# Kernel optimization log

Measured on AMD Instinct MI355X. Metric: run time of the kernel, lower is better.

The kernel has to match this reference:

```python
import jax, jax.numpy as jnp
import numpy as np

B, S, H, NH = 2, 2048, 1024, 16
DK = H // NH

def setup_inputs() -> dict:
    key = jax.random.key(0)
    ks = jax.random.split(key, 12)
    scale = 0.02
    return {
        "Q": jax.random.normal(ks[0], (B, S, H), jnp.float32),
        "K": jax.random.normal(ks[1], (B, S, H), jnp.float32),
        "V": jax.random.normal(ks[2], (B, S, H), jnp.float32),
        "attn_mask": jax.random.randint(ks[3], (B, S, S), 0, 2).astype(bool),
        "Wq": jax.random.normal(ks[4], (H, H), jnp.float32) * scale,
        "bq": jnp.zeros((H,), jnp.float32),
        "Wk": jax.random.normal(ks[5], (H, H), jnp.float32) * scale,
        "bk": jnp.zeros((H,), jnp.float32),
        "Wv": jax.random.normal(ks[6], (H, H), jnp.float32) * scale,
        "bv": jnp.zeros((H,), jnp.float32),
        "Wo": jax.random.normal(ks[7], (H, H), jnp.float32) * scale,
        "bo": jnp.zeros((H,), jnp.float32),
    }

def reference(Q, K, V, attn_mask, Wq, bq, Wk, bk, Wv, bv, Wo, bo):
    b = Q.shape[0]
    # linear projections (torch nn.Linear: x @ W.T + b), split heads -> [b, nh, s, dk]
    def proj(x, W, bias):
        return (x @ W.T + bias).reshape(b, -1, NH, DK).transpose(0, 2, 1, 3)
    q = proj(Q, Wq, bq)
    k = proj(K, Wk, bk)
    v = proj(V, Wv, bv)
    scores = jnp.einsum("bhqd,bhkd->bhqk", q, k) / jnp.sqrt(jnp.float32(DK))
    scores = jnp.where(attn_mask[:, None, :, :], jnp.float32(-1e9), scores)
    attn = jax.nn.softmax(scores, axis=-1)  # dropout prob = 0.0 (identity)
    ctx = jnp.einsum("bhqk,bhkd->bhqd", attn, v)
    ctx = ctx.transpose(0, 2, 1, 3).reshape(b, -1, NH * DK)
    return ctx @ Wo.T + bo
```

## Files before the change

kernel.cpp:

```cpp
#include <hip/hip_runtime.h>
#include <hip/hip_bf16.h>

typedef short s16x8 __attribute__((ext_vector_type(8)));
typedef float f32x4 __attribute__((ext_vector_type(4)));
typedef unsigned short u16;
typedef unsigned int u32;
typedef unsigned long long u64;

#define DEVI __device__ __forceinline__

#if __has_builtin(__builtin_amdgcn_exp2f)
#define EXP2F(x) __builtin_amdgcn_exp2f(x)
#else
#define EXP2F(x) exp2f(x)
#endif

#define QSCALE 0.1803368801111204f

DEVI float bf2f(u16 u){ union { u32 i; float f; } v; v.i = ((u32)u) << 16; return v.f; }
DEVI u16 f2bf(float f){ union { float f; u32 i; } v; v.f = f; u32 u = v.i;
                        return (u16)((u + 0x7fffu + ((u >> 16) & 1u)) >> 16); }

DEVI u32 pkbf2(float a, float b){
  union { __hip_bfloat162 h; u32 u; } v;
  v.h = __float22bfloat162_rn(make_float2(a, b));
  return v.u;
}
DEVI u64 pk4(float a, float b, float c, float d){
  return (u64)pkbf2(a, b) | ((u64)pkbf2(c, d) << 32);
}

DEVI f32x4 mfma_bf16(s16x8 a, s16x8 b, f32x4 c){
  return __builtin_amdgcn_mfma_f32_16x16x32_bf16(a, b, c, 0, 0, 0);
}

#define GLDS(gp, lp) __builtin_amdgcn_global_load_lds( \
    (const __attribute__((address_space(1))) void*)(gp), \
    (__attribute__((address_space(3))) void*)(lp), 16, 0, 0)

DEVI float4 cvt8f32(const float* p){
  float4 x = *(const float4*)p;
  float4 y = *(const float4*)(p + 4);
  union { u32 t[4]; float4 f4; } u;
  u.t[0] = pkbf2(x.x, x.y); u.t[1] = pkbf2(x.z, x.w);
  u.t[2] = pkbf2(y.x, y.y); u.t[3] = pkbf2(y.z, y.w);
  return u.f4;
}

DEVI bool detect_f32(const u16* probe){
  __shared__ int dsum[4];
  const int tid = threadIdx.x;
  int bad = 0;
#pragma unroll
  for (int i = 0; i < 16; ++i){
    u16 u = probe[tid * 16 + i];
    int e = (u >> 7) & 0xFF;
    bad += (e != 0 && (e < 100 || e > 150)) ? 1 : 0;
  }
#pragma unroll
  for (int o = 1; o < 64; o <<= 1) bad += __shfl_xor(bad, o);
  if ((tid & 63) == 0) dsum[tid >> 6] = bad;
  __syncthreads();
  bool r = (dsum[0] + dsum[1] + dsum[2] + dsum[3]) > 64;
  __syncthreads();
  return r;
}

struct PrepArgs { const void* src[7]; void* dst[7]; u32 coff[8]; };

__global__ __launch_bounds__(256) void prep_mask(PrepArgs a, const u16* probe,
                                                 const int* __restrict__ mask,
                                                 u64* __restrict__ bits,
                                                 int do_mask, int do_conv){
  if (blockIdx.x < 1024){
    if (!do_mask) return;
    const int lane = threadIdx.x & 63, wid = threadIdx.x >> 6;
    const int row = blockIdx.x * 4 + wid;
    const int* mrow = mask + (size_t)row * 2048;
    for (int c = 0; c < 32; ++c){
      int v = mrow[c * 64 + lane];
      u64 w = __ballot(v == 0);
      if (lane == 0) bits[(size_t)row * 32 + c] = w;
    }
  } else {
    if (!do_conv) return;
    const bool f32 = detect_f32(probe);
    if (!f32) return;
    const u32 total = a.coff[7];
    for (u32 c = (blockIdx.x - 1024) * 256 + threadIdx.x; c < total; c += 2048 * 256){
      int s = 0;
#pragma unroll
      for (int i = 1; i < 7; ++i) s += (c >= a.coff[i]) ? 1 : 0;
      u32 lc = c - a.coff[s];
      ((float4*)a.dst[s])[lc] = cvt8f32((const float*)a.src[s] + (size_t)lc * 8);
    }
  }
}

struct ProjP {
  const void* X[3];   const u16* Xc[3];
  const void* W[3];   const u16* Wc[3];
  const void* bias[3];
  u16* out[3];
  const u16* probe;
  int conv_ok;
};

__global__ __launch_bounds__(256) void proj_gemm(ProjP p){
  __shared__ u16 As[128 * 64];
  __shared__ u16 Bs[128 * 64];
  const int z = blockIdx.z;
  const bool in32 = detect_f32(p.probe);
  const bool f32st = in32 && !p.conv_ok;
  const u16* Ab = (in32 && p.conv_ok) ? p.Xc[z] : (const u16*)p.X[z];
  const u16* Wb = (in32 && p.conv_ok) ? p.Wc[z] : (const u16*)p.W[z];
  const float* Af = (const float*)p.X[z];
  const float* Wf = (const float*)p.W[z];
  const int tid = threadIdx.x;
  const int lane = tid & 63, wid = tid >> 6;
  const int quad = lane >> 4, l15 = lane & 15;
  const int m0 = blockIdx.y * 128, n0 = blockIdx.x * 128;
  const int wm = (wid >> 1) * 64, wn = (wid & 1) * 64;
  const int K = 1024;

  f32x4 acc[4][4];
  const f32x4 z4 = {0.f, 0.f, 0.f, 0.f};
  for (int i = 0; i < 4; ++i) for (int j = 0; j < 4; ++j) acc[i][j] = z4;

  for (int ko = 0; ko < 16; ++ko){
    const int kk = ko * 64;
    if (f32st){
#pragma unroll
      for (int i = 0; i < 4; ++i){
        int g = tid * 4 + i;
        int row = g >> 3, c = g & 7;
        *(float4*)(As + row * 64 + ((c ^ (row & 7)) * 8)) =
            cvt8f32(Af + (size_t)(m0 + row) * K + kk + c * 8);
        *(float4*)(Bs + row * 64 + ((c ^ (row & 7)) * 8)) =
            cvt8f32(Wf + (size_t)(n0 + row) * K + kk + c * 8);
      }
    } else {
#pragma unroll
      for (int i = 0; i < 4; ++i){
        int ci = (wid * 4 + i) * 64 + lane;
        int row = ci >> 3, gcc = (ci & 7) ^ (row & 7);
        GLDS(Ab + (size_t)(m0 + row) * K + kk + gcc * 8, As + (size_t)(wid * 4 + i) * 512);
        GLDS(Wb + (size_t)(n0 + row) * K + kk + gcc * 8, Bs + (size_t)(wid * 4 + i) * 512);
      }
    }
    __syncthreads();
#pragma unroll
    for (int ks = 0; ks < 2; ++ks){
      s16x8 af[4], bfr[4];
#pragma unroll
      for (int mt = 0; mt < 4; ++mt){
        int row = wm + mt * 16 + l15;
        af[mt] = *(const s16x8*)(As + row * 64 + (((ks * 4 + quad) ^ (row & 7)) * 8));
      }
#pragma unroll
      for (int nt = 0; nt < 4; ++nt){
        int row = wn + nt * 16 + l15;
        bfr[nt] = *(const s16x8*)(Bs + row * 64 + (((ks * 4 + quad) ^ (row & 7)) * 8));
      }
#pragma unroll
      for (int mt = 0; mt < 4; ++mt)
#pragma unroll
        for (int nt = 0; nt < 4; ++nt)
          acc[mt][nt] = mfma_bf16(af[mt], bfr[nt], acc[mt][nt]);
    }
    __syncthreads();
  }

  u16* outp = p.out[z];
#pragma unroll
  for (int nt = 0; nt < 4; ++nt){
    int col = n0 + wn + nt * 16 + l15;
    float bv = in32 ? ((const float*)p.bias[z])[col] : bf2f(((const u16*)p.bias[z])[col]);
#pragma unroll
    for (int mt = 0; mt < 4; ++mt){
      if (z == 2){
        int srow = m0 + wm + mt * 16 + quad * 4;
        int b = srow >> 11, s = srow & 2047, hh = col >> 6, d = col & 63;
        size_t idx = (((size_t)(b * 16 + hh)) * 64 + d) * 2048 + s;
        *(u64*)(outp + idx) = pk4(acc[mt][nt][0] + bv, acc[mt][nt][1] + bv,
                                  acc[mt][nt][2] + bv, acc[mt][nt][3] + bv);
      } else {
#pragma unroll
        for (int r = 0; r < 4; ++r){
          int row = m0 + wm + mt * 16 + quad * 4 + r;
          float v = acc[mt][nt][r] + bv;
          if (z == 0) v *= QSCALE;
          int b = row >> 11, s = row & 2047, hh = col >> 6, d = col & 63;
          outp[(((size_t)(b * 16 + hh)) * 2048 + s) * 64 + d] = f2bf(v);
        }
      }
    }
  }
}

__global__ __launch_bounds__(256) void gemm_out(const u16* __restrict__ A,
                                                const void* __restrict__ Wv,
                                                const u16* __restrict__ Wbf,
                                                const void* __restrict__ biasv,
                                                void* __restrict__ outv,
                                                const u16* __restrict__ probe,
                                                int conv_ok){
  __shared__ u16 As[64 * 64];
  __shared__ u16 Bs[64 * 64];
  const bool in32 = detect_f32(probe);
  const bool f32st = in32 && !conv_ok;
  const u16* Wb = (in32 && conv_ok) ? Wbf : (const u16*)Wv;
  const float* Wf = (const float*)Wv;
  const int tid = threadIdx.x;
  const int lane = tid & 63, wid = tid >> 6;
  const int quad = lane >> 4, l15 = lane & 15;
  const int m0 = blockIdx.y * 64, n0 = blockIdx.x * 64;
  const int wm = (wid >> 1) * 32, wn = (wid & 1) * 32;
  const int K = 1024;

  f32x4 acc[2][2];
  const f32x4 z4 = {0.f, 0.f, 0.f, 0.f};
  for (int i = 0; i < 2; ++i) for (int j = 0; j < 2; ++j) acc[i][j] = z4;

  for (int ko = 0; ko < 16; ++ko){
    const int kk = ko * 64;
#pragma unroll
    for (int i = 0; i < 2; ++i){
      int ci = (wid * 2 + i) * 64 + lane;
      int row = ci >> 3, gcc = (ci & 7) ^ (row & 7);
      GLDS(A + (size_t)(m0 + row) * K + kk + gcc * 8, As + (size_t)(wid * 2 + i) * 512);
    }
    if (f32st){
#pragma unroll
      for (int i = 0; i < 2; ++i){
        int g = tid * 2 + i;
        int row = g >> 3, c = g & 7;
        *(float4*)(Bs + row * 64 + ((c ^ (row & 7)) * 8)) =
            cvt8f32(Wf + (size_t)(n0 + row) * K + kk + c * 8);
      }
    } else {
#pragma unroll
      for (int i = 0; i < 2; ++i){
        int ci = (wid * 2 + i) * 64 + lane;
        int row = ci >> 3, gcc = (ci & 7) ^ (row & 7);
        GLDS(Wb + (size_t)(n0 + row) * K + kk + gcc * 8, Bs + (size_t)(wid * 2 + i) * 512);
      }
    }
    __syncthreads();
#pragma unroll
    for (int ks = 0; ks < 2; ++ks){
      s16x8 af[2], bfr[2];
#pragma unroll
      for (int mt = 0; mt < 2; ++mt){
        int row = wm + mt * 16 + l15;
        af[mt] = *(const s16x8*)(As + row * 64 + (((ks * 4 + quad) ^ (row & 7)) * 8));
      }
#pragma unroll
      for (int nt = 0; nt < 2; ++nt){
        int row = wn + nt * 16 + l15;
        bfr[nt] = *(const s16x8*)(Bs + row * 64 + (((ks * 4 + quad) ^ (row & 7)) * 8));
      }
#pragma unroll
      for (int mt = 0; mt < 2; ++mt)
#pragma unroll
        for (int nt = 0; nt < 2; ++nt)
          acc[mt][nt] = mfma_bf16(af[mt], bfr[nt], acc[mt][nt]);
    }
    __syncthreads();
  }

#pragma unroll
  for (int nt = 0; nt < 2; ++nt){
    int col = n0 + wn + nt * 16 + l15;
    float bv = in32 ? ((const float*)biasv)[col] : bf2f(((const u16*)biasv)[col]);
#pragma unroll
    for (int mt = 0; mt < 2; ++mt)
#pragma unroll
      for (int r = 0; r < 4; ++r){
        int row = m0 + wm + mt * 16 + quad * 4 + r;
        float v = acc[mt][nt][r] + bv;
        size_t idx = (size_t)row * 1024 + col;
        if (in32) ((float*)outv)[idx] = v;
        else      ((u16*)outv)[idx]   = f2bf(v);
      }
  }
}

__global__ __launch_bounds__(256) void attn2(const u16* __restrict__ qws,
                                             const u16* __restrict__ kws,
                                             const u16* __restrict__ vtws,
                                             const u64* __restrict__ mbits,
                                             const int* __restrict__ rawmask,
                                             int use_raw,
                                             u16* __restrict__ ctxws){
  __shared__ u16 Ks[2][64 * 64];
  __shared__ u16 Vt[2][64 * 64];
  __shared__ u16 Ps[4][16 * 64];
  const int tid = threadIdx.x;
  const int lane = tid & 63, wid = tid >> 6;
  const int quad = lane >> 4, l15 = lane & 15;
  const int h = blockIdx.x, qt = blockIdx.y, b = blockIdx.z;
  const int q0 = qt * 64;
  const size_t bh = (size_t)(b * 16 + h) * (2048 * 64);
  const int qrow = q0 + wid * 16 + l15;

  s16x8 qf[2];
#pragma unroll
  for (int ks = 0; ks < 2; ++ks)
    qf[ks] = *(const s16x8*)(qws + bh + (size_t)qrow * 64 + ks * 32 + quad * 8);

  const f32x4 z4 = {0.f, 0.f, 0.f, 0.f};
  f32x4 ctx[4];
  for (int dt = 0; dt < 4; ++dt) ctx[dt] = z4;
  float lr = 0.f;

  u16* pp = &Ps[wid][0];
  u32 pw[4];
#pragma unroll
  for (int ntk = 0; ntk < 4; ++ntk)
    pw[ntk] = l15 * 64 + (((u32)(ntk * 2 + (quad >> 1)) ^ (u32)(l15 & 7)) * 8) + (quad & 1) * 4;

  const u64* mrow = mbits + ((size_t)(b * 2048 + qrow)) * 32;

  const int sci = wid * 2;
  int srow0, sgc0, srow1, sgc1;
  {
    int ci0 = sci * 64 + lane;
    srow0 = ci0 >> 3; sgc0 = (ci0 & 7) ^ (srow0 & 7);
    int ci1 = (sci + 1) * 64 + lane;
    srow1 = ci1 >> 3; sgc1 = (ci1 & 7) ^ (srow1 & 7);
  }

  {
    const int k0 = 0;
    GLDS(kws + bh + (size_t)(k0 + srow0) * 64 + sgc0 * 8, &Ks[0][0] + (size_t)sci * 512);
    GLDS(vtws + bh + (size_t)srow0 * 2048 + k0 + sgc0 * 8, &Vt[0][0] + (size_t)sci * 512);
    GLDS(kws + bh + (size_t)(k0 + srow1) * 64 + sgc1 * 8, &Ks[0][0] + (size_t)(sci + 1) * 512);
    GLDS(vtws + bh + (size_t)srow1 * 2048 + k0 + sgc1 * 8, &Vt[0][0] + (size_t)(sci + 1) * 512);
  }

  for (int kt = 0; kt < 32; ++kt){
    const int cur = kt & 1;
    const u16* kb = &Ks[cur][0];
    const u16* vb = &Vt[cur][0];
    __syncthreads();

    u64 mw = 0;
    if (!use_raw) mw = mrow[kt];

    if (kt < 31){
      const int k0n = (kt + 1) * 64;
      u16* kd = &Ks[cur ^ 1][0];
      u16* vd = &Vt[cur ^ 1][0];
      GLDS(kws + bh + (size_t)(k0n + srow0) * 64 + sgc0 * 8, kd + (size_t)sci * 512);
      GLDS(vtws + bh + (size_t)srow0 * 2048 + k0n + sgc0 * 8, vd + (size_t)sci * 512);
      GLDS(kws + bh + (size_t)(k0n + srow1) * 64 + sgc1 * 8, kd + (size_t)(sci + 1) * 512);
      GLDS(vtws + bh + (size_t)srow1 * 2048 + k0n + sgc1 * 8, vd + (size_t)(sci + 1) * 512);
    }

    const int k0 = kt * 64;

    f32x4 s[4];
    for (int ntk = 0; ntk < 4; ++ntk) s[ntk] = z4;
#pragma unroll
    for (int ks = 0; ks < 2; ++ks)
#pragma unroll
      for (int ntk = 0; ntk < 4; ++ntk){
        int row = ntk * 16 + l15;
        s16x8 kf = *(const s16x8*)(kb + row * 64 + (((ks * 4 + quad) ^ (row & 7)) * 8));
        s[ntk] = mfma_bf16(kf, qf[ks], s[ntk]);
      }

    float ls = 0.f;
    if (!use_raw){
      u64 w = mw >> (quad * 4);
      u32 wlo = (u32)w, whi = (u32)(w >> 32);
#pragma unroll
      for (int ntk = 0; ntk < 4; ++ntk){
        u32 half = (ntk < 2) ? wlo : whi;
#pragma unroll
        for (int r = 0; r < 4; ++r){
          u32 keep = half & (1u << ((ntk & 1) * 16 + r));
          float sv = keep ? s[ntk][r] : -1.0e9f;
          float pv = EXP2F(sv);
          s[ntk][r] = pv;
          ls += pv;
        }
      }
    } else {
#pragma unroll
      for (int ntk = 0; ntk < 4; ++ntk)
#pragma unroll
        for (int r = 0; r < 4; ++r){
          int key = k0 + ntk * 16 + quad * 4 + r;
          int mv = rawmask[((size_t)(b * 2048 + qrow)) * 2048 + key];
          float pv = EXP2F(mv ? -1.0e9f : s[ntk][r]);
          s[ntk][r] = pv;
          ls += pv;
        }
    }
    lr += ls;

#pragma unroll
    for (int ntk = 0; ntk < 4; ++ntk){
      uint2 t;
      t.x = pkbf2(s[ntk][0], s[ntk][1]);
      t.y = pkbf2(s[ntk][2], s[ntk][3]);
      *(uint2*)(pp + pw[ntk]) = t;
    }
    s16x8 pf[2];
#pragma unroll
    for (int ks = 0; ks < 2; ++ks)
      pf[ks] = *(const s16x8*)(pp + l15 * 64 + (((ks * 4 + quad) ^ (l15 & 7)) * 8));

#pragma unroll
    for (int ks = 0; ks < 2; ++ks)
#pragma unroll
      for (int dt = 0; dt < 4; ++dt){
        int row = dt * 16 + l15;
        s16x8 vf = *(const s16x8*)(vb + row * 64 + (((ks * 4 + quad) ^ (row & 7)) * 8));
        ctx[dt] = mfma_bf16(vf, pf[ks], ctx[dt]);
      }
  }

  lr += __shfl_xor(lr, 16);
  lr += __shfl_xor(lr, 32);
  float inv = 1.0f / fmaxf(lr, 1e-30f);

#pragma unroll
  for (int dt = 0; dt < 4; ++dt){
    int d0 = dt * 16 + quad * 4;
    u64 w = pk4(ctx[dt][0] * inv, ctx[dt][1] * inv, ctx[dt][2] * inv, ctx[dt][3] * inv);
    *(u64*)(ctxws + ((size_t)(b * 2048 + qrow)) * 1024 + h * 64 + d0) = w;
  }
}

extern "C" void kernel_launch(void* const* d_in, const int* in_sizes, int n_in,
                              void* d_out, int out_size, void* d_ws, size_t ws_size,
                              hipStream_t stream){
  const void* Q    = d_in[0];
  const void* Kin  = d_in[1];
  const void* Vin  = d_in[2];
  const int* mask  = (const int*)d_in[3];
  const void* Wq = d_in[4];  const void* bq = d_in[5];
  const void* Wk = d_in[6];  const void* bk = d_in[7];
  const void* Wv = d_in[8];  const void* bv = d_in[9];
  const void* Wo = d_in[10]; const void* bo = d_in[11];

  char* ws = (char*)d_ws;
  const size_t MB = 1u << 20;
  const bool small_ws = ws_size < 33 * MB;
  const bool big_ws   = ws_size >= 66 * MB;
  u64* mbits = (u64*)ws;
  const size_t base = small_ws ? 0 : MB;
  u16* qws  = (u16*)(ws + base);
  u16* kws  = (u16*)(ws + base + 8 * MB);
  u16* vtws = (u16*)(ws + base + 16 * MB);
  u16* cws  = (u16*)(ws + base + 24 * MB);
  u16* Qc  = (u16*)(ws + 33 * MB);
  u16* Kc  = (u16*)(ws + 41 * MB);
  u16* Vc  = (u16*)(ws + 49 * MB);
  u16* Wqc = (u16*)(ws + 57 * MB);
  u16* Wkc = (u16*)(ws + 59 * MB);
  u16* Wvc = (u16*)(ws + 61 * MB);
  u16* Woc = (u16*)(ws + 63 * MB);
  const u16* probe = (const u16*)Q;

  PrepArgs pa;
  pa.src[0] = Q;  pa.src[1] = Kin; pa.src[2] = Vin;
  pa.src[3] = Wq; pa.src[4] = Wk;  pa.src[5] = Wv; pa.src[6] = Wo;
  pa.dst[0] = Qc;  pa.dst[1] = Kc;  pa.dst[2] = Vc;
  pa.dst[3] = Wqc; pa.dst[4] = Wkc; pa.dst[5] = Wvc; pa.dst[6] = Woc;
  const u32 cq = 4194304 / 8, cw = 1048576 / 8;
  pa.coff[0] = 0;
  pa.coff[1] = cq;          pa.coff[2] = 2 * cq;      pa.coff[3] = 3 * cq;
  pa.coff[4] = 3 * cq + cw; pa.coff[5] = 3 * cq + 2 * cw;
  pa.coff[6] = 3 * cq + 3 * cw; pa.coff[7] = 3 * cq + 4 * cw;
  prep_mask<<<dim3(3072), 256, 0, stream>>>(pa, probe, mask, mbits,
                                            small_ws ? 0 : 1, big_ws ? 1 : 0);

  ProjP pp;
  pp.X[0] = Q;  pp.X[1] = Kin; pp.X[2] = Vin;
  pp.Xc[0] = Qc; pp.Xc[1] = Kc; pp.Xc[2] = Vc;
  pp.W[0] = Wq; pp.W[1] = Wk; pp.W[2] = Wv;
  pp.Wc[0] = Wqc; pp.Wc[1] = Wkc; pp.Wc[2] = Wvc;
  pp.bias[0] = bq; pp.bias[1] = bk; pp.bias[2] = bv;
  pp.out[0] = qws; pp.out[1] = kws; pp.out[2] = vtws;
  pp.probe = probe;
  pp.conv_ok = big_ws ? 1 : 0;
  proj_gemm<<<dim3(8, 32, 3), 256, 0, stream>>>(pp);

  attn2<<<dim3(16, 32, 2), 256, 0, stream>>>(qws, kws, vtws, mbits, mask,
                                             small_ws ? 1 : 0, cws);

  gemm_out<<<dim3(16, 64), 256, 0, stream>>>(cws, Wo, Woc, bo, d_out, probe,
                                             big_ws ? 1 : 0);
}
```

Measured before the change: 276.2 us.

## Process two query row groups per warp to reuse K/V tiles in attention

Each attention block now covers 128 query rows instead of 64, with each warp handling two 16-row groups. Each K and V fragment read from shared memory then feeds two MFMAs, halving K/V global and LDS traffic per query row. The launch grid is halved and launch bounds request two blocks per CU. The kt loop is manually unrolled by the double buffer, and global pointers are advanced incrementally. The cost is higher register pressure and fewer blocks (512) to fill the GPU.

```diff
diff --git a/kernel.cpp b/kernel.cpp
--- a/kernel.cpp
+++ b/kernel.cpp
@@ -286,41 +286,51 @@
   }
 }
 
-__global__ __launch_bounds__(256) void attn2(const u16* __restrict__ qws,
-                                             const u16* __restrict__ kws,
-                                             const u16* __restrict__ vtws,
-                                             const u64* __restrict__ mbits,
-                                             const int* __restrict__ rawmask,
-                                             int use_raw,
-                                             u16* __restrict__ ctxws){
+__global__ __launch_bounds__(256, 2) void attn2(const u16* __restrict__ qws,
+                                                const u16* __restrict__ kws,
+                                                const u16* __restrict__ vtws,
+                                                const u64* __restrict__ mbits,
+                                                const int* __restrict__ rawmask,
+                                                int use_raw,
+                                                u16* __restrict__ ctxws){
   __shared__ u16 Ks[2][64 * 64];
   __shared__ u16 Vt[2][64 * 64];
-  __shared__ u16 Ps[4][16 * 64];
+  __shared__ u16 Ps[4][32 * 64];
   const int tid = threadIdx.x;
   const int lane = tid & 63, wid = tid >> 6;
   const int quad = lane >> 4, l15 = lane & 15;
   const int h = blockIdx.x, qt = blockIdx.y, b = blockIdx.z;
-  const int q0 = qt * 64;
+  const int q0 = qt * 128;
   const size_t bh = (size_t)(b * 16 + h) * (2048 * 64);
-  const int qrow = q0 + wid * 16 + l15;
-
-  s16x8 qf[2];
-#pragma unroll
-  for (int ks = 0; ks < 2; ++ks)
-    qf[ks] = *(const s16x8*)(qws + bh + (size_t)qrow * 64 + ks * 32 + quad * 8);
+  int qrow[2];
+  qrow[0] = q0 + wid * 32 + l15;
+  qrow[1] = qrow[0] + 16;
+
+  s16x8 qf[2][2];
+#pragma unroll
+  for (int rg = 0; rg < 2; ++rg)
+#pragma unroll
+    for (int ks = 0; ks < 2; ++ks)
+      qf[rg][ks] = *(const s16x8*)(qws + bh + (size_t)qrow[rg] * 64 + ks * 32 + quad * 8);
 
   const f32x4 z4 = {0.f, 0.f, 0.f, 0.f};
-  f32x4 ctx[4];
-  for (int dt = 0; dt < 4; ++dt) ctx[dt] = z4;
-  float lr = 0.f;
+  f32x4 ctx[2][4];
+#pragma unroll
+  for (int rg = 0; rg < 2; ++rg)
+    for (int dt = 0; dt < 4; ++dt) ctx[rg][dt] = z4;
+  float lr[2] = {0.f, 0.f};
 
   u16* pp = &Ps[wid][0];
-  u32 pw[4];
-#pragma unroll
-  for (int ntk = 0; ntk < 4; ++ntk)
-    pw[ntk] = l15 * 64 + (((u32)(ntk * 2 + (quad >> 1)) ^ (u32)(l15 & 7)) * 8) + (quad & 1) * 4;
-
-  const u64* mrow = mbits + ((size_t)(b * 2048 + qrow)) * 32;
+  u32 pw[2][4];
+#pragma unroll
+  for (int rg = 0; rg < 2; ++rg)
+#pragma unroll
+    for (int ntk = 0; ntk < 4; ++ntk)
+      pw[rg][ntk] = (rg * 16 + l15) * 64 +
+                    (((u32)(ntk * 2 + (quad >> 1)) ^ (u32)(l15 & 7)) * 8) + (quad & 1) * 4;
+
+  const u64* mrow0 = mbits + ((size_t)(b * 2048 + qrow[0])) * 32;
+  const u64* mrow1 = mbits + ((size_t)(b * 2048 + qrow[1])) * 32;
 
   const int sci = wid * 2;
   int srow0, sgc0, srow1, sgc1;
@@ -330,108 +340,133 @@
     int ci1 = (sci + 1) * 64 + lane;
     srow1 = ci1 >> 3; sgc1 = (ci1 & 7) ^ (srow1 & 7);
   }
-
-  {
-    const int k0 = 0;
-    GLDS(kws + bh + (size_t)(k0 + srow0) * 64 + sgc0 * 8, &Ks[0][0] + (size_t)sci * 512);
-    GLDS(vtws + bh + (size_t)srow0 * 2048 + k0 + sgc0 * 8, &Vt[0][0] + (size_t)sci * 512);
-    GLDS(kws + bh + (size_t)(k0 + srow1) * 64 + sgc1 * 8, &Ks[0][0] + (size_t)(sci + 1) * 512);
-    GLDS(vtws + bh + (size_t)srow1 * 2048 + k0 + sgc1 * 8, &Vt[0][0] + (size_t)(sci + 1) * 512);
-  }
-
-  for (int kt = 0; kt < 32; ++kt){
-    const int cur = kt & 1;
-    const u16* kb = &Ks[cur][0];
-    const u16* vb = &Vt[cur][0];
-    __syncthreads();
-
-    u64 mw = 0;
-    if (!use_raw) mw = mrow[kt];
-
-    if (kt < 31){
-      const int k0n = (kt + 1) * 64;
-      u16* kd = &Ks[cur ^ 1][0];
-      u16* vd = &Vt[cur ^ 1][0];
-      GLDS(kws + bh + (size_t)(k0n + srow0) * 64 + sgc0 * 8, kd + (size_t)sci * 512);
-      GLDS(vtws + bh + (size_t)srow0 * 2048 + k0n + sgc0 * 8, vd + (size_t)sci * 512);
-      GLDS(kws + bh + (size_t)(k0n + srow1) * 64 + sgc1 * 8, kd + (size_t)(sci + 1) * 512);
-      GLDS(vtws + bh + (size_t)srow1 * 2048 + k0n + sgc1 * 8, vd + (size_t)(sci + 1) * 512);
-    }
-
-    const int k0 = kt * 64;
-
-    f32x4 s[4];
-    for (int ntk = 0; ntk < 4; ++ntk) s[ntk] = z4;
-#pragma unroll
-    for (int ks = 0; ks < 2; ++ks)
-#pragma unroll
-      for (int ntk = 0; ntk < 4; ++ntk){
-        int row = ntk * 16 + l15;
-        s16x8 kf = *(const s16x8*)(kb + row * 64 + (((ks * 4 + quad) ^ (row & 7)) * 8));
-        s[ntk] = mfma_bf16(kf, qf[ks], s[ntk]);
-      }
-
-    float ls = 0.f;
-    if (!use_raw){
-      u64 w = mw >> (quad * 4);
-      u32 wlo = (u32)w, whi = (u32)(w >> 32);
-#pragma unroll
-      for (int ntk = 0; ntk < 4; ++ntk){
-        u32 half = (ntk < 2) ? wlo : whi;
-#pragma unroll
-        for (int r = 0; r < 4; ++r){
-          u32 keep = half & (1u << ((ntk & 1) * 16 + r));
-          float sv = keep ? s[ntk][r] : -1.0e9f;
-          float pv = EXP2F(sv);
-          s[ntk][r] = pv;
-          ls += pv;
+  const u16* kp0 = kws + bh + (size_t)srow0 * 64 + sgc0 * 8;
+  const u16* kp1 = kws + bh + (size_t)srow1 * 64 + sgc1 * 8;
+  const u16* vp0 = vtws + bh + (size_t)srow0 * 2048 + sgc0 * 8;
+  const u16* vp1 = vtws + bh + (size_t)srow1 * 2048 + sgc1 * 8;
+
+  GLDS(kp0, &Ks[0][0] + (size_t)sci * 512);
+  GLDS(vp0, &Vt[0][0] + (size_t)sci * 512);
+  GLDS(kp1, &Ks[0][0] + (size_t)(sci + 1) * 512);
+  GLDS(vp1, &Vt[0][0] + (size_t)(sci + 1) * 512);
+  kp0 += 4096; kp1 += 4096; vp0 += 64; vp1 += 64;
+
+  for (int kt = 0; kt < 32; kt += 2){
+#pragma unroll
+    for (int hb = 0; hb < 2; ++hb){
+      const int t = kt + hb;
+      const u16* kb = &Ks[hb][0];
+      const u16* vb = &Vt[hb][0];
+      __syncthreads();
+
+      u64 mw0 = 0, mw1 = 0;
+      if (!use_raw){ mw0 = mrow0[t]; mw1 = mrow1[t]; }
+
+      if (t < 31){
+        u16* kd = &Ks[hb ^ 1][0];
+        u16* vd = &Vt[hb ^ 1][0];
+        GLDS(kp0, kd + (size_t)sci * 512);
+        GLDS(vp0, vd + (size_t)sci * 512);
+        GLDS(kp1, kd + (size_t)(sci + 1) * 512);
+        GLDS(vp1, vd + (size_t)(sci + 1) * 512);
+        kp0 += 4096; kp1 += 4096; vp0 += 64; vp1 += 64;
+      }
+
+      f32x4 s[2][4];
+#pragma unroll
+      for (int rg = 0; rg < 2; ++rg)
+#pragma unroll
+        for (int ntk = 0; ntk < 4; ++ntk) s[rg][ntk] = z4;
+#pragma unroll
+      for (int ks = 0; ks < 2; ++ks)
+#pragma unroll
+        for (int ntk = 0; ntk < 4; ++ntk){
+          int row = ntk * 16 + l15;
+          s16x8 kf = *(const s16x8*)(kb + row * 64 + (((ks * 4 + quad) ^ (row & 7)) * 8));
+          s[0][ntk] = mfma_bf16(kf, qf[0][ks], s[0][ntk]);
+          s[1][ntk] = mfma_bf16(kf, qf[1][ks], s[1][ntk]);
         }
-      }
-    } else {
-#pragma unroll
-      for (int ntk = 0; ntk < 4; ++ntk)
-#pragma unroll
-        for (int r = 0; r < 4; ++r){
-          int key = k0 + ntk * 16 + quad * 4 + r;
-          int mv = rawmask[((size_t)(b * 2048 + qrow)) * 2048 + key];
-          float pv = EXP2F(mv ? -1.0e9f : s[ntk][r]);
-          s[ntk][r] = pv;
-          ls += pv;
+
+      if (!use_raw){
+#pragma unroll
+        for (int rg = 0; rg < 2; ++rg){
+          u64 w = (rg ? mw1 : mw0) >> (quad * 4);
+          u32 wlo = (u32)w, whi = (u32)(w >> 32);
+          float ls = 0.f;
+#pragma unroll
+          for (int ntk = 0; ntk < 4; ++ntk){
+            u32 half32 = (ntk < 2) ? wlo : whi;
+#pragma unroll
+            for (int r = 0; r < 4; ++r){
+              u32 keep = half32 & (1u << ((ntk & 1) * 16 + r));
+              float sv = keep ? s[rg][ntk][r] : -1.0e9f;
+              float pv = EXP2F(sv);
+              s[rg][ntk][r] = pv;
+              ls += pv;
+            }
+          }
+          lr[rg] += ls;
         }
-    }
-    lr += ls;
-
-#pragma unroll
-    for (int ntk = 0; ntk < 4; ++ntk){
-      uint2 t;
-      t.x = pkbf2(s[ntk][0], s[ntk][1]);
-      t.y = pkbf2(s[ntk][2], s[ntk][3]);
-      *(uint2*)(pp + pw[ntk]) = t;
-    }
-    s16x8 pf[2];
-#pragma unroll
-    for (int ks = 0; ks < 2; ++ks)
-      pf[ks] = *(const s16x8*)(pp + l15 * 64 + (((ks * 4 + quad) ^ (l15 & 7)) * 8));
-
-#pragma unroll
-    for (int ks = 0; ks < 2; ++ks)
-#pragma unroll
-      for (int dt = 0; dt < 4; ++dt){
-        int row = dt * 16 + l15;
-        s16x8 vf = *(const s16x8*)(vb + row * 64 + (((ks * 4 + quad) ^ (row & 7)) * 8));
-        ctx[dt] = mfma_bf16(vf, pf[ks], ctx[dt]);
-      }
-  }
-
-  lr += __shfl_xor(lr, 16);
-  lr += __shfl_xor(lr, 32);
-  float inv = 1.0f / fmaxf(lr, 1e-30f);
-
-#pragma unroll
-  for (int dt = 0; dt < 4; ++dt){
-    int d0 = dt * 16 + quad * 4;
-    u64 w = pk4(ctx[dt][0] * inv, ctx[dt][1] * inv, ctx[dt][2] * inv, ctx[dt][3] * inv);
-    *(u64*)(ctxws + ((size_t)(b * 2048 + qrow)) * 1024 + h * 64 + d0) = w;
+      } else {
+        const int k0 = t * 64;
+#pragma unroll
+        for (int rg = 0; rg < 2; ++rg){
+          float ls = 0.f;
+#pragma unroll
+          for (int ntk = 0; ntk < 4; ++ntk)
+#pragma unroll
+            for (int r = 0; r < 4; ++r){
+              int key = k0 + ntk * 16 + quad * 4 + r;
+              int mv = rawmask[((size_t)(b * 2048 + qrow[rg])) * 2048 + key];
+              float pv = EXP2F(mv ? -1.0e9f : s[rg][ntk][r]);
+              s[rg][ntk][r] = pv;
+              ls += pv;
+            }
+          lr[rg] += ls;
+        }
+      }
+
+#pragma unroll
+      for (int rg = 0; rg < 2; ++rg)
+#pragma unroll
+        for (int ntk = 0; ntk < 4; ++ntk){
+          uint2 tt;
+          tt.x = pkbf2(s[rg][ntk][0], s[rg][ntk][1]);
+          tt.y = pkbf2(s[rg][ntk][2], s[rg][ntk][3]);
+          *(uint2*)(pp + pw[rg][ntk]) = tt;
+        }
+      s16x8 pf[2][2];
+#pragma unroll
+      for (int rg = 0; rg < 2; ++rg)
+#pragma unroll
+        for (int ks = 0; ks < 2; ++ks)
+          pf[rg][ks] = *(const s16x8*)(pp + (rg * 16 + l15) * 64 +
+                                       (((ks * 4 + quad) ^ (l15 & 7)) * 8));
+
+#pragma unroll
+      for (int ks = 0; ks < 2; ++ks)
+#pragma unroll
+        for (int dt = 0; dt < 4; ++dt){
+          int row = dt * 16 + l15;
+          s16x8 vf = *(const s16x8*)(vb + row * 64 + (((ks * 4 + quad) ^ (row & 7)) * 8));
+          ctx[0][dt] = mfma_bf16(vf, pf[0][ks], ctx[0][dt]);
+          ctx[1][dt] = mfma_bf16(vf, pf[1][ks], ctx[1][dt]);
+        }
+    }
+  }
+
+#pragma unroll
+  for (int rg = 0; rg < 2; ++rg){
+    lr[rg] += __shfl_xor(lr[rg], 16);
+    lr[rg] += __shfl_xor(lr[rg], 32);
+    float inv = 1.0f / fmaxf(lr[rg], 1e-30f);
+#pragma unroll
+    for (int dt = 0; dt < 4; ++dt){
+      int d0 = dt * 16 + quad * 4;
+      u64 w = pk4(ctx[rg][dt][0] * inv, ctx[rg][dt][1] * inv,
+                  ctx[rg][dt][2] * inv, ctx[rg][dt][3] * inv);
+      *(u64*)(ctxws + ((size_t)(b * 2048 + qrow[rg])) * 1024 + h * 64 + d0) = w;
+    }
   }
 }
 
@@ -490,7 +525,7 @@
   pp.conv_ok = big_ws ? 1 : 0;
   proj_gemm<<<dim3(8, 32, 3), 256, 0, stream>>>(pp);
 
-  attn2<<<dim3(16, 32, 2), 256, 0, stream>>>(qws, kws, vtws, mbits, mask,
+  attn2<<<dim3(16, 16, 2), 256, 0, stream>>>(qws, kws, vtws, mbits, mask,
                                              small_ws ? 1 : 0, cws);
 
   gemm_out<<<dim3(16, 64), 256, 0, stream>>>(cws, Wo, Woc, bo, d_out, probe,
```

Result: no change. 279.7 us (+1.3%).
